# Kernel optimization log

Hardware: AMD Instinct MI355X
Metric: run time of the kernel (lower is better)

Reference implementation:

```python
import jax, jax.numpy as jnp
import numpy as np

N, E, D, R, L = 100000, 800000, 64, 7, 3
HID, KH = D // 4, 32          # IEConv hidden = dims[i]//4, kernel_hidden_dim = 32
EDGE_DIM = 14
BN_EPS = 1e-5
LN_EPS = 1e-5


def _normalize(v, eps=1e-12):
    n = jnp.linalg.norm(v, axis=-1, keepdims=True)
    return v / jnp.maximum(n, eps)


def _bn(h, p):
    # eval-mode BatchNorm1d; p: [4, dim] = (gamma, beta, running_mean, running_var)
    return (h - p[2]) * jax.lax.rsqrt(p[3] + BN_EPS) * p[0] + p[1]


def setup_inputs() -> dict:
    key = jax.random.key(0)
    keys = iter(jax.random.split(key, 40))
    nk = lambda: next(keys)
    par = lambda shape, s=0.1: jax.random.normal(nk(), shape, jnp.float32) * s

    def bn_par(dim):
        g = 1.0 + 0.1 * jax.random.normal(nk(), (L, dim), jnp.float32)
        b = 0.1 * jax.random.normal(nk(), (L, dim), jnp.float32)
        m = 0.1 * jax.random.normal(nk(), (L, dim), jnp.float32)
        v = 0.5 + jax.random.uniform(nk(), (L, dim), jnp.float32)
        return jnp.stack([g, b, m, v], axis=1)  # [L,4,dim]

    inp = {
        "x": jax.random.normal(nk(), (N, D), jnp.float32),
        "pos": jax.random.normal(nk(), (N, 3), jnp.float32) * 10.0,
        "edge_index": jax.random.randint(nk(), (2, E), 0, N),
        "edge_relation": jax.random.randint(nk(), (E,), 0, R),
        # GeometricRelationalGraphConv params (per layer)
        "W_rel": par((L, R * D, D)), "b_rel": par((L, D)),
        "W_self": par((L, D, D)), "b_self": par((L, D)),
        # IEConvLayer params
        "W_l1": par((L, D, HID)), "b_l1": par((L, HID)),
        "W_k1": par((L, EDGE_DIM, KH)), "b_k1": par((L, KH)),
        "W_k2": par((L, KH, (HID + 1) * HID)), "b_k2": par((L, (HID + 1) * HID)),
        "W_l2": par((L, HID, D)), "b_l2": par((L, D)),
        "bn_in": bn_par(D), "bn_msg": bn_par(HID), "bn_upd": bn_par(HID), "bn_out": bn_par(D),
        "ln_g": 1.0 + 0.1 * jax.random.normal(nk(), (L, D), jnp.float32),
        "ln_b": 0.1 * jax.random.normal(nk(), (L, D), jnp.float32),
    }
    return inp


def _forward(x, pos, W_rel, b_rel, W_self, b_self, W_l1, b_l1, W_k1, b_k1,
             W_k2, b_k2, W_l2, b_l2, bn_in, bn_msg, bn_upd, bn_out, ln_g, ln_b,
             edge_index, edge_relation):
    node_in, node_out = edge_index[0], edge_index[1]
    # ---- get_ieconv_edge_feature ----
    ones3 = jnp.ones((1, 3), x.dtype)
    u = _normalize(jnp.concatenate([ones3, pos[1:] - pos[:-1]], axis=0))        # [N,3]
    b = _normalize(jnp.concatenate([u[:-1] - u[1:], ones3], axis=0))
    n = _normalize(jnp.concatenate([jnp.cross(u[:-1], u[1:]), ones3], axis=0))
    frame = jnp.stack([b, n, jnp.cross(b, n)], axis=-1)                          # [N,3,3]
    t = jnp.einsum('ejk,ej->ek', frame[node_in], pos[node_out] - pos[node_in])  # [E,3]
    r = jnp.sum(frame[node_in] * frame[node_out], axis=1)                        # [E,3]
    delta = (jnp.abs(node_in - node_out).astype(x.dtype) / 6.0)[:, None]         # atom2residue = arange
    edge_feat = jnp.concatenate(
        [t, r, delta, 1 - 2 * jnp.abs(t), 1 - 2 * jnp.abs(r), 1 - 2 * jnp.abs(delta)], axis=-1)  # [E,14]

    deg = jnp.maximum(
        jax.ops.segment_sum(jnp.ones_like(node_out, dtype=x.dtype), node_out, num_segments=N), 1.0)[:, None]
    seg = node_out * R + edge_relation
    h = x
    for i in range(L):
        # GeometricRelationalGraphConv: relation-bucketed scatter-sum, per-relation linear + self loop, relu
        upd = jax.ops.segment_sum(h[node_in], seg, num_segments=N * R).reshape(N, R * h.shape[-1])
        rel_out = jax.nn.relu(upd @ W_rel[i] + b_rel[i] + h @ W_self[i] + b_self[i])
        # IEConvLayer (eval mode, dropouts identity)
        li = jax.nn.relu(_bn(h, bn_in[i]))
        m = jax.nn.relu(_bn(li[node_in] @ W_l1[i] + b_l1[i], bn_msg[i]))         # [E,HID]
        ker = (jax.nn.relu(edge_feat @ W_k1[i] + b_k1[i]) @ W_k2[i] + b_k2[i]).reshape(-1, HID + 1, HID)
        m = jnp.einsum('ejk,ej->ek', ker[:, 1:, :], m) + ker[:, 0, :]            # per-edge kernel conv
        upd2 = jax.ops.segment_sum(m, node_out, num_segments=N) / deg            # scatter-mean
        upd2 = jax.nn.relu(_bn(upd2, bn_upd[i]))
        ie_out = _bn(upd2 @ W_l2[i] + b_l2[i], bn_out[i])
        hidden = rel_out + ie_out + h  # short_cut: shapes match at every layer
        mu = jnp.mean(hidden, axis=-1, keepdims=True)
        var = jnp.var(hidden, axis=-1, keepdims=True)
        h = (hidden - mu) * jax.lax.rsqrt(var + LN_EPS) * ln_g[i] + ln_b[i]
    return h


def reference(x, pos, edge_index, edge_relation, W_rel, b_rel, W_self, b_self,
              W_l1, b_l1, W_k1, b_k1, W_k2, b_k2, W_l2, b_l2,
              bn_in, bn_msg, bn_upd, bn_out, ln_g, ln_b):
    return _forward(x, pos, W_rel, b_rel, W_self, b_self, W_l1, b_l1, W_k1, b_k1,
                    W_k2, b_k2, W_l2, b_l2, bn_in, bn_msg, bn_upd, bn_out, ln_g, ln_b,
                    edge_index, edge_relation)
```

## Files before the change

### kernel.cpp

```cpp
#include <hip/hip_runtime.h>
#include <hip/hip_bf16.h>

typedef unsigned short u16;
typedef unsigned int   u32;

static const int Nn  = 100000;
static const int Ne  = 800000;
static const int Ll  = 3;
static const int SCAN_B = 98;

typedef short     short8  __attribute__((ext_vector_type(8)));
typedef float     floatx4 __attribute__((ext_vector_type(4)));

static const int H_CUM[19] = {
  0, 86016, 86208, 98496, 98688, 101760, 101808, 103152, 103248,
  129360, 130176, 133248, 133440, 134208, 134400, 134592, 135360, 135552, 135744
};
static const int H_SZ[18] = {
  86016, 192, 12288, 192, 3072, 48, 1344, 96,
  26112, 816, 3072, 192, 768, 192, 192, 768, 192, 192
};

union FU { u32 u; float f; };
__device__ __forceinline__ float b2f(u16 v) { FU x; x.u = ((u32)v) << 16; return x.f; }
__device__ __forceinline__ float lo2f(u32 w) { FU x; x.u = w << 16; return x.f; }
__device__ __forceinline__ float hi2f(u32 w) { FU x; x.u = w & 0xffff0000u; return x.f; }
__device__ __forceinline__ u16 f2b(float f) {
  FU x; x.f = f;
  u32 u = x.u;
  u32 r = (u + 0x7FFFu + ((u >> 16) & 1u)) >> 16;
  return (u16)r;
}
__device__ __forceinline__ u32 pk2(float a, float b) {
  __hip_bfloat162 h2 = __float22bfloat162_rn(make_float2(a, b));
  union { __hip_bfloat162 h; u32 u; } c; c.h = h2; return c.u;
}

__global__ void k_bnprep(const float* __restrict__ W, float* __restrict__ bnAB) {
  int idx = blockIdx.x * blockDim.x + threadIdx.x;
  if (idx >= 480) return;
  int i = idx / 160, d0 = idx % 160;
  const float* src; float* dstA; float* dstB; int dim, d;
  if (d0 < 64)       { d = d0;      src = W + 133440 + i * 256; dim = 64; dstA = bnAB + i*320 + 0;   dstB = bnAB + i*320 + 64;  }
  else if (d0 < 80)  { d = d0 - 64; src = W + 134208 + i * 64;  dim = 16; dstA = bnAB + i*320 + 128; dstB = bnAB + i*320 + 144; }
  else if (d0 < 96)  { d = d0 - 80; src = W + 134400 + i * 64;  dim = 16; dstA = bnAB + i*320 + 160; dstB = bnAB + i*320 + 176; }
  else               { d = d0 - 96; src = W + 134592 + i * 256; dim = 64; dstA = bnAB + i*320 + 192; dstB = bnAB + i*320 + 256; }
  float g = src[0*dim+d], b = src[1*dim+d], m = src[2*dim+d], v = src[3*dim+d];
  float A = g * rsqrtf(v + 1e-5f);
  float B = b - m * A;
  dstA[d] = A; dstB[d] = B;
}

__global__ void k_prep(const float* __restrict__ W, u16* __restrict__ BswG) {
  int i = blockIdx.x * 256 + threadIdx.x;
  if (i >= 3 * 8704) return;
  int layer = i / 8704, r = i % 8704;
  int jp = r / 512, l2 = r % 512;
  int lane = l2 / 8, j = l2 % 8;
  int q = (lane >> 4) * 8 + j, n = lane & 15;
  const float* Wk2 = W + 103248 + layer * 8704;
  BswG[i] = f2b(Wk2[q * 272 + jp * 16 + n]);
}

__global__ void k_prep2(const float* __restrict__ W, u16* __restrict__ B2) {
  int idx = blockIdx.x * 256 + threadIdx.x;
  if (idx >= 3 * 65536) return;
  int layer = idx >> 16, r = idx & 65535;
  int fr = r >> 9;
  int lane = (r >> 3) & 63, j = r & 7;
  int hl = fr & 1, ks = (fr >> 1) & 1, nt = (fr >> 2) & 3, nc = fr >> 4;
  int k = ks * 32 + (lane >> 4) * 8 + j;
  int g = nc * 64 + nt * 16 + (lane & 15);
  const float* Wrel  = W + layer * 28672;
  const float* Wself = W + 86208 + layer * 4096;
  float v = (g < 448) ? Wrel[((g >> 6) * 64 + k) * 64 + (g & 63)]
                      : Wself[k * 64 + (g - 448)];
  u16 hi = f2b(v);
  B2[idx] = hl ? f2b(v - b2f(hi)) : hi;
}

__global__ void k_u(const float* __restrict__ posf, float* __restrict__ u) {
  int i = blockIdx.x * blockDim.x + threadIdx.x;
  if (i >= Nn) return;
  float ux, uy, uz;
  if (i == 0) { ux = uy = uz = 0.57735026918962584f; }
  else {
    float vx = posf[i*3+0] - posf[(i-1)*3+0];
    float vy = posf[i*3+1] - posf[(i-1)*3+1];
    float vz = posf[i*3+2] - posf[(i-1)*3+2];
    float nrm = sqrtf(vx*vx + vy*vy + vz*vz);
    float inv = 1.0f / fmaxf(nrm, 1e-12f);
    ux = vx*inv; uy = vy*inv; uz = vz*inv;
  }
  u[i*3+0] = ux; u[i*3+1] = uy; u[i*3+2] = uz;
}

__global__ void k_frame(const float* __restrict__ u, float* __restrict__ frame) {
  int i = blockIdx.x * blockDim.x + threadIdx.x;
  if (i >= Nn) return;
  float bx, by, bz, nx, ny, nz;
  if (i < Nn - 1) {
    float ax = u[i*3+0], ay = u[i*3+1], az = u[i*3+2];
    float cx = u[(i+1)*3+0], cy = u[(i+1)*3+1], cz = u[(i+1)*3+2];
    float dx = ax-cx, dy = ay-cy, dz = az-cz;
    float n1 = sqrtf(dx*dx + dy*dy + dz*dz);
    float i1 = 1.0f / fmaxf(n1, 1e-12f);
    bx = dx*i1; by = dy*i1; bz = dz*i1;
    float qx = ay*cz - az*cy, qy = az*cx - ax*cz, qz = ax*cy - ay*cx;
    float n2 = sqrtf(qx*qx + qy*qy + qz*qz);
    float i2 = 1.0f / fmaxf(n2, 1e-12f);
    nx = qx*i2; ny = qy*i2; nz = qz*i2;
  } else {
    bx = by = bz = 0.57735026918962584f;
    nx = ny = nz = 0.57735026918962584f;
  }
  float ex = by*nz - bz*ny, ey = bz*nx - bx*nz, ez = bx*ny - by*nx;
  frame[i*9+0] = bx; frame[i*9+1] = nx; frame[i*9+2] = ex;
  frame[i*9+3] = by; frame[i*9+4] = ny; frame[i*9+5] = ey;
  frame[i*9+6] = bz; frame[i*9+7] = nz; frame[i*9+8] = ez;
}

__global__ void k_edge(const int* __restrict__ EI, const float* __restrict__ posf,
                       const float* __restrict__ frame,
                       float* __restrict__ t0, float* __restrict__ t1, float* __restrict__ t2,
                       float* __restrict__ r0, float* __restrict__ r1, float* __restrict__ r2,
                       int* __restrict__ cnt) {
  int e = blockIdx.x * 256 + threadIdx.x;
  int vin = EI[e], vout = EI[Ne + e];
  float fi[9], fo[9];
#pragma unroll
  for (int t = 0; t < 9; t++) fi[t] = frame[(size_t)vin*9 + t];
#pragma unroll
  for (int t = 0; t < 9; t++) fo[t] = frame[(size_t)vout*9 + t];
  float d0 = posf[vout*3+0] - posf[vin*3+0];
  float d1 = posf[vout*3+1] - posf[vin*3+1];
  float d2 = posf[vout*3+2] - posf[vin*3+2];
  float tt[3], rr[3];
#pragma unroll
  for (int k = 0; k < 3; k++) {
    tt[k] = fi[0*3+k]*d0 + fi[1*3+k]*d1 + fi[2*3+k]*d2;
    rr[k] = fi[0*3+k]*fo[0*3+k] + fi[1*3+k]*fo[1*3+k] + fi[2*3+k]*fo[2*3+k];
  }
  t0[e] = tt[0]; t1[e] = tt[1]; t2[e] = tt[2];
  r0[e] = rr[0]; r1[e] = rr[1]; r2[e] = rr[2];
  atomicAdd(&cnt[vout], 1);
}

__global__ __launch_bounds__(1024) void k_scan1(const int* __restrict__ cnt,
                                                int* __restrict__ locExc,
                                                int* __restrict__ btot) {
  __shared__ int sm[1024];
  int t = threadIdx.x, b = blockIdx.x;
  int i = b * 1024 + t;
  int v = (i < Nn) ? cnt[i] : 0;
  sm[t] = v;
  __syncthreads();
#pragma unroll
  for (int off = 1; off < 1024; off <<= 1) {
    int x = (t >= off) ? sm[t - off] : 0;
    __syncthreads();
    sm[t] += x;
    __syncthreads();
  }
  if (i < Nn) locExc[i] = sm[t] - v;
  if (t == 1023) btot[b] = sm[1023];
}

__global__ void k_scan2(const int* __restrict__ btot, int* __restrict__ boff,
                        int* __restrict__ rowptr) {
  if (threadIdx.x != 0 || blockIdx.x != 0) return;
  int run = 0;
  for (int b = 0; b < SCAN_B; b++) { boff[b] = run; run += btot[b]; }
  rowptr[Nn] = run;
}

__global__ void k_scan3(const int* __restrict__ cnt, const int* __restrict__ locExc,
                        const int* __restrict__ boff, int* __restrict__ rowptr,
                        float* __restrict__ deginv) {
  int i = blockIdx.x * blockDim.x + threadIdx.x;
  if (i >= Nn) return;
  rowptr[i] = locExc[i] + boff[i >> 10];
  int dv = cnt[i] > 1 ? cnt[i] : 1;
  deginv[i] = 1.0f / (float)dv;
}

__global__ void k_place(const int* __restrict__ EI, const int* __restrict__ EREL,
                        const int* __restrict__ rowptr,
                        int* __restrict__ fill, int* __restrict__ yidx,
                        int* __restrict__ inv) {
  int e = blockIdx.x * blockDim.x + threadIdx.x;
  if (e >= Ne) return;
  int vout = EI[Ne + e];
  int p = atomicAdd(&fill[vout], 1);
  int slot = rowptr[vout] + p;
  inv[e] = slot;
  yidx[slot] = EI[e] * 448 + EREL[e] * 64;
}

__global__ __launch_bounds__(256) void k_rel2(
    const float* __restrict__ h, const u16* __restrict__ Bsw,
    const float* __restrict__ brel, const float* __restrict__ bself,
    u16* __restrict__ Y, u16* __restrict__ S) {
  __shared__ uint4 bs4[1024];
  int tid = threadIdx.x;
  int w = tid >> 6, lane = tid & 63;
  int kq = lane >> 4, cl = lane & 15;
  int nb0 = blockIdx.x * 64;
  int anode = nb0 + w * 16 + cl;
  union U { uint4 u; short8 v; };

  uint4 Ah[2], Al[2];
#pragma unroll
  for (int ks = 0; ks < 2; ks++) {
    float p[8] = {0.f,0.f,0.f,0.f,0.f,0.f,0.f,0.f};
    if (anode < Nn) {
      const float4* hp = (const float4*)(h + (size_t)anode * 64 + ks * 32 + kq * 8);
      float4 q0 = hp[0], q1 = hp[1];
      p[0]=q0.x; p[1]=q0.y; p[2]=q0.z; p[3]=q0.w;
      p[4]=q1.x; p[5]=q1.y; p[6]=q1.z; p[7]=q1.w;
    }
    u32 hw[4], lw[4];
#pragma unroll
    for (int t = 0; t < 4; t++) {
      u16 ha = f2b(p[2*t]), hb = f2b(p[2*t+1]);
      hw[t] = (u32)ha | ((u32)hb << 16);
      lw[t] = pk2(p[2*t] - b2f(ha), p[2*t+1] - b2f(hb));
    }
    Ah[ks] = make_uint4(hw[0], hw[1], hw[2], hw[3]);
    Al[ks] = make_uint4(lw[0], lw[1], lw[2], lw[3]);
  }

  for (int nc = 0; nc < 8; nc++) {
    if (nc) __syncthreads();
    const uint4* src = (const uint4*)(Bsw + nc * 8192);
#pragma unroll
    for (int i = 0; i < 4; i++) bs4[tid + i * 256] = src[tid + i * 256];
    __syncthreads();

    floatx4 acc[4];
#pragma unroll
    for (int nt = 0; nt < 4; nt++) acc[nt] = (floatx4){0.f, 0.f, 0.f, 0.f};
#pragma unroll
    for (int nt = 0; nt < 4; nt++) {
#pragma unroll
      for (int ks = 0; ks < 2; ks++) {
        U bh, bl, ah, al;
        bh.u = bs4[((nt*2 + ks)*2 + 0)*64 + lane];
        bl.u = bs4[((nt*2 + ks)*2 + 1)*64 + lane];
        ah.u = Ah[ks]; al.u = Al[ks];
        acc[nt] = __builtin_amdgcn_mfma_f32_16x16x32_bf16(ah.v, bh.v, acc[nt], 0, 0, 0);
        acc[nt] = __builtin_amdgcn_mfma_f32_16x16x32_bf16(al.v, bh.v, acc[nt], 0, 0, 0);
        acc[nt] = __builtin_amdgcn_mfma_f32_16x16x32_bf16(ah.v, bl.v, acc[nt], 0, 0, 0);
      }
    }
    if (nc < 7) {
#pragma unroll
      for (int nt = 0; nt < 4; nt++) {
#pragma unroll
        for (int reg = 0; reg < 4; reg++) {
          int node = nb0 + w * 16 + kq * 4 + reg;
          if (node < Nn)
            Y[(size_t)node * 448 + nc * 64 + nt * 16 + cl] = f2b(acc[nt][reg]);
        }
      }
    } else {
#pragma unroll
      for (int nt = 0; nt < 4; nt++) {
        int c = nt * 16 + cl;
        float bias = brel[c] + bself[c];
#pragma unroll
        for (int reg = 0; reg < 4; reg++) {
          int node = nb0 + w * 16 + kq * 4 + reg;
          if (node < Nn)
            S[(size_t)node * 64 + c] = f2b(acc[nt][reg] + bias);
        }
      }
    }
  }
}

__global__ __launch_bounds__(256) void k_z(
    const float* __restrict__ h, const float* __restrict__ Wl1, const float* __restrict__ bl1,
    const float* __restrict__ bk2, const float* __restrict__ bn,
    u16* __restrict__ zt, u16* __restrict__ biast) {
  __shared__ float ls[64][65];
  __shared__ float zz[64][17];
  int tid = threadIdx.x;
  int nb0 = blockIdx.x * 64;
  const float* Ain = bn + 0;
  const float* Bin = bn + 64;
#pragma unroll
  for (int r = 0; r < 16; r++) {
    int idx = r * 256 + tid;
    int row = idx >> 6, col = idx & 63;
    int node = nb0 + row;
    float v = (node < Nn) ? h[(size_t)node * 64 + col] : 0.0f;
    ls[row][col] = fmaxf(v * Ain[col] + Bin[col], 0.0f);
  }
  __syncthreads();
  int row = tid >> 2, jq = (tid & 3) * 4;
  int node = nb0 + row;
  const float* Amsg = bn + 128;
  const float* Bmsg = bn + 144;
  float m1[4];
#pragma unroll
  for (int t = 0; t < 4; t++) m1[t] = bl1[jq + t];
  for (int c = 0; c < 64; c++) {
    float lv = ls[row][c];
#pragma unroll
    for (int t = 0; t < 4; t++) m1[t] += lv * Wl1[c * 16 + jq + t];
  }
  float zv[4];
#pragma unroll
  for (int t = 0; t < 4; t++) {
    zv[t] = fmaxf(m1[t] * Amsg[jq + t] + Bmsg[jq + t], 0.0f);
    zz[row][jq + t] = zv[t];
  }
  if (node < Nn) {
    u32* zg = (u32*)zt + (size_t)node * 8 + (tid & 3) * 2;
    zg[0] = pk2(zv[0], zv[1]);
    zg[1] = pk2(zv[2], zv[3]);
  }
  __syncthreads();
  float bb[4];
#pragma unroll
  for (int t = 0; t < 4; t++) bb[t] = bk2[jq + t];
  for (int j = 0; j < 16; j++) {
    float zj = zz[row][j];
#pragma unroll
    for (int t = 0; t < 4; t++) bb[t] += zj * bk2[(j + 1) * 16 + jq + t];
  }
  if (node < Nn) {
    u32* bg = (u32*)biast + (size_t)node * 8 + (tid & 3) * 2;
    bg[0] = pk2(bb[0], bb[1]);
    bg[1] = pk2(bb[2], bb[3]);
  }
}

__global__ __launch_bounds__(256) void k_msg(
    const float* __restrict__ t0, const float* __restrict__ t1, const float* __restrict__ t2,
    const float* __restrict__ r0, const float* __restrict__ r1, const float* __restrict__ r2,
    const int* __restrict__ EI, const int* __restrict__ inv,
    const u16* __restrict__ zt, const u16* __restrict__ biast,
    const float* __restrict__ Wk1, const float* __restrict__ bk1,
    const u16* __restrict__ BswG, u16* __restrict__ mo) {
  __shared__ u16 abuf[256 * 72];
  __shared__ u32 bsw[4352];

  int tid = threadIdx.x;
  int e0 = blockIdx.x * 256;
  int e = e0 + tid;

  for (int i = tid; i < 4352; i += 256) bsw[i] = ((const u32*)BswG)[i];

  int vin = EI[e], vout = EI[Ne + e];

  {
    const uint4* zg = (const uint4*)(zt + (size_t)vin * 16);
    uint4* zr = (uint4*)(abuf + (size_t)tid * 72 + 32);
    zr[0] = zg[0]; zr[1] = zg[1];
    const uint4* bg = (const uint4*)(biast + (size_t)vin * 16);
    uint4* br = (uint4*)(abuf + (size_t)tid * 72 + 48);
    br[0] = bg[0]; br[1] = bg[1];
  }

  float ef[14];
  ef[0] = t0[e]; ef[1] = t1[e]; ef[2] = t2[e];
  ef[3] = r0[e]; ef[4] = r1[e]; ef[5] = r2[e];
  int ad = vin - vout; if (ad < 0) ad = -ad;
  ef[6] = ((float)ad) / 6.0f;
#pragma unroll
  for (int k = 0; k < 7; k++) ef[7+k] = 1.0f - 2.0f*fabsf(ef[k]);

  float a[32];
#pragma unroll
  for (int q = 0; q < 32; q++) a[q] = bk1[q];
#pragma unroll
  for (int d = 0; d < 14; d++) {
    float fv = ef[d];
#pragma unroll
    for (int q = 0; q < 32; q++) a[q] += fv * Wk1[d*32 + q];
  }
  u32* ar = (u32*)(abuf + (size_t)tid * 72);
#pragma unroll
  for (int q = 0; q < 16; q++)
    ar[q] = pk2(fmaxf(a[2*q], 0.0f), fmaxf(a[2*q+1], 0.0f));
  __syncthreads();

  int lane = tid & 63, w4 = (tid >> 6) * 4;
  int m = lane & 15, quad = lane >> 4;
  union U { uint4 u; short8 v; };
#pragma unroll
  for (int t = 0; t < 4; t++) {
    int s0 = (w4 + t) * 16;
    int s = s0 + m;
    const u16* rs = abuf + (size_t)s * 72;
    U afr;
    afr.u = *(const uint4*)(rs + quad * 8);
    const u32* aw = (const u32*)&afr.u;
    float av[8];
#pragma unroll
    for (int j = 0; j < 4; j++) { av[2*j] = lo2f(aw[j]); av[2*j+1] = hi2f(aw[j]); }

    uint4 zu0 = *(const uint4*)(rs + 32);
    uint4 zu1 = *(const uint4*)(rs + 40);
    const u32* zw0 = (const u32*)&zu0;
    const u32* zw1 = (const u32*)&zu1;
    float zf[16];
#pragma unroll
    for (int j = 0; j < 4; j++) {
      zf[2*j]   = lo2f(zw0[j]); zf[2*j+1]   = hi2f(zw0[j]);
      zf[8+2*j] = lo2f(zw1[j]); zf[8+2*j+1] = hi2f(zw1[j]);
    }

    floatx4 acc = {0.0f, 0.0f, 0.0f, 0.0f};
    U bfr;
    bfr.u = *(const uint4*)(bsw + (size_t)(0 * 64 + lane) * 4);
    acc = __builtin_amdgcn_mfma_f32_16x16x32_bf16(afr.v, bfr.v, acc, 0, 0, 0);

#pragma unroll
    for (int jp = 1; jp < 17; jp++) {
      float zv = zf[jp - 1];
      U pf;
      u32* pw = (u32*)&pf.u;
#pragma unroll
      for (int j = 0; j < 4; j++)
        pw[j] = pk2(av[2*j] * zv, av[2*j+1] * zv);
      bfr.u = *(const uint4*)(bsw + (size_t)(jp * 64 + lane) * 4);
      acc = __builtin_amdgcn_mfma_f32_16x16x32_bf16(pf.v, bfr.v, acc, 0, 0, 0);
    }

    int k = m;
#pragma unroll
    for (int reg = 0; reg < 4; reg++) {
      int se = s0 + quad * 4 + reg;
      float bias = b2f(abuf[(size_t)se * 72 + 48 + k]);
      int slot = inv[e0 + se];
      mo[(size_t)slot * 16 + k] = f2b(acc[reg] + bias);
    }
  }
}

__global__ __launch_bounds__(256) void k_node(
    const float* __restrict__ h, const u16* __restrict__ S, const u16* __restrict__ Y,
    const int* __restrict__ rowptr, const int* __restrict__ yidx,
    const u16* __restrict__ mo, const float* __restrict__ deginv,
    const float* __restrict__ Wl2, const float* __restrict__ bl2,
    const float* __restrict__ bn, const float* __restrict__ lng, const float* __restrict__ lnb,
    float* __restrict__ hout) {
  __shared__ float relsm[4][64];
  __shared__ float u2s[4][16];
  int tid = threadIdx.x;
  int lane = tid & 63, w = tid >> 6;
  int n = blockIdx.x * 4 + w;
  bool act = (n < Nn);

  if (act) {
    int beg = rowptr[n], end = rowptr[n+1];

    int g = lane >> 4, col4 = lane & 15;
    float a4[4] = {0.f, 0.f, 0.f, 0.f};
    for (int c0 = beg; c0 < end; c0 += 64) {
      int l = c0 + lane;
      int yo = (l < end) ? yidx[l] : 0;
      int cnt = end - c0; if (cnt > 64) cnt = 64;
      for (int j0 = 0; j0 < cnt; j0 += 4) {
        int j = j0 + g;
        int yoj = __shfl(yo, j, 64);
        if (j < cnt) {
          uint2 d = *(const uint2*)(Y + (size_t)yoj + col4 * 4);
          a4[0] += lo2f(d.x); a4[1] += hi2f(d.x);
          a4[2] += lo2f(d.y); a4[3] += hi2f(d.y);
        }
      }
    }
#pragma unroll
    for (int t = 0; t < 4; t++) {
      a4[t] += __shfl_xor(a4[t], 16, 64);
      a4[t] += __shfl_xor(a4[t], 32, 64);
    }
    if (lane < 16) {
#pragma unroll
      for (int t = 0; t < 4; t++) relsm[w][col4 * 4 + t] = a4[t];
    }

    int r = lane >> 2, c4 = lane & 3;
    float p4[4] = {0.f, 0.f, 0.f, 0.f};
    for (int p0 = beg; p0 < end; p0 += 16) {
      int p = p0 + r;
      if (p < end) {
        uint2 d = *(const uint2*)(mo + (size_t)p * 16 + c4 * 4);
        p4[0] += lo2f(d.x); p4[1] += hi2f(d.x);
        p4[2] += lo2f(d.y); p4[3] += hi2f(d.y);
      }
    }
#pragma unroll
    for (int t = 0; t < 4; t++) {
      p4[t] += __shfl_xor(p4[t],  4, 64);
      p4[t] += __shfl_xor(p4[t],  8, 64);
      p4[t] += __shfl_xor(p4[t], 16, 64);
      p4[t] += __shfl_xor(p4[t], 32, 64);
    }
    const float* Aupd = bn + 160;
    const float* Bupd = bn + 176;
    if (lane < 4) {
      float di = deginv[n];
#pragma unroll
      for (int t = 0; t < 4; t++) {
        int col = c4 * 4 + t;
        float v = p4[t] * di;
        u2s[w][col] = fmaxf(v * Aupd[col] + Bupd[col], 0.0f);
      }
    }
  }
  __syncthreads();
  if (act) {
    float rel_out = fmaxf(b2f(S[(size_t)n*64 + lane]) + relsm[w][lane], 0.0f);
    float ie = bl2[lane];
#pragma unroll
    for (int j = 0; j < 16; j++) ie += u2s[w][j] * Wl2[j*64 + lane];
    const float* Aout = bn + 192;
    const float* Bout = bn + 256;
    ie = ie * Aout[lane] + Bout[lane];
    float hidden = rel_out + ie + h[(size_t)n*64 + lane];
    float s = hidden;
#pragma unroll
    for (int off = 32; off > 0; off >>= 1) s += __shfl_xor(s, off, 64);
    float mu = s * (1.0f/64.0f);
    float d = hidden - mu;
    float s2 = d * d;
#pragma unroll
    for (int off = 32; off > 0; off >>= 1) s2 += __shfl_xor(s2, off, 64);
    float var = s2 * (1.0f/64.0f);
    float o = d * rsqrtf(var + 1e-5f) * lng[lane] + lnb[lane];
    hout[(size_t)n*64 + lane] = o;
  }
}

extern "C" void kernel_launch(void* const* d_in, const int* in_sizes, int n_in,
                              void* d_out, int out_size, void* d_ws, size_t ws_size,
                              hipStream_t stream) {
  const float* x    = (const float*)d_in[0];
  const float* posf = (const float*)d_in[1];
  const int* EI     = (const int*)d_in[2];
  const int* EREL   = (const int*)d_in[3];
  float* outf       = (float*)d_out;

  char* p = (char*)d_ws;
  auto alloc = [&](size_t bytes) -> char* {
    char* r = p;
    p += (bytes + 255) & ~((size_t)255);
    return r;
  };
  float* W      = (float*)alloc((size_t)135744 * 4);
  float* bnAB   = (float*)alloc((size_t)960 * 4);
  u16*   BswG   = (u16*)  alloc((size_t)3 * 8704 * 2);
  u16*   Bsw2   = (u16*)  alloc((size_t)3 * 65536 * 2);
  float* u      = (float*)alloc((size_t)Nn * 3 * 4);
  float* frame  = (float*)alloc((size_t)Nn * 9 * 4);
  int*   cnt    = (int*)  alloc((size_t)Nn * 4);
  int*   fill   = (int*)  alloc((size_t)Nn * 4);
  int*   rowptr = (int*)  alloc((size_t)(Nn + 1) * 4);
  int*   locExc = (int*)  alloc((size_t)Nn * 4);
  int*   btot   = (int*)  alloc((size_t)SCAN_B * 4);
  int*   boff   = (int*)  alloc((size_t)SCAN_B * 4);
  int*   yidx   = (int*)  alloc((size_t)Ne * 4);
  int*   inv    = (int*)  alloc((size_t)Ne * 4);
  float* deginv = (float*)alloc((size_t)Nn * 4);
  float* h      = (float*)alloc((size_t)Nn * 64 * 4);
  u16*   S      = (u16*)  alloc((size_t)Nn * 64 * 2);
  u16*   Y      = (u16*)  alloc((size_t)Nn * 448 * 2);
  u16*   mo     = (u16*)  alloc((size_t)Ne * 16 * 2);
  u16*   zt     = (u16*)  alloc((size_t)Nn * 16 * 2);
  u16*   biast  = (u16*)  alloc((size_t)Nn * 16 * 2);
  float* et0    = (float*)alloc((size_t)Ne * 4);
  float* et1    = (float*)alloc((size_t)Ne * 4);
  float* et2    = (float*)alloc((size_t)Ne * 4);
  float* er0    = (float*)alloc((size_t)Ne * 4);
  float* er1    = (float*)alloc((size_t)Ne * 4);
  float* er2    = (float*)alloc((size_t)Ne * 4);
  (void)n_in; (void)in_sizes; (void)out_size;

  size_t needed = (size_t)(p - (char*)d_ws);
  if (needed > ws_size) return;

  hipMemsetAsync(cnt,  0, (size_t)Nn * 4, stream);
  hipMemsetAsync(fill, 0, (size_t)Nn * 4, stream);

  for (int k = 0; k < 18; k++)
    hipMemcpyAsync(W + H_CUM[k], d_in[4 + k], (size_t)H_SZ[k] * 4,
                   hipMemcpyDeviceToDevice, stream);
  hipMemcpyAsync(h, x, (size_t)Nn * 64 * 4, hipMemcpyDeviceToDevice, stream);

  k_bnprep<<<2, 256, 0, stream>>>(W, bnAB);
  k_prep<<<(3*8704 + 255)/256, 256, 0, stream>>>(W, BswG);
  k_prep2<<<(3*65536 + 255)/256, 256, 0, stream>>>(W, Bsw2);
  k_u<<<(Nn + 255)/256, 256, 0, stream>>>(posf, u);
  k_frame<<<(Nn + 255)/256, 256, 0, stream>>>(u, frame);
  k_edge<<<Ne/256, 256, 0, stream>>>(EI, posf, frame, et0, et1, et2, er0, er1, er2, cnt);
  k_scan1<<<SCAN_B, 1024, 0, stream>>>(cnt, locExc, btot);
  k_scan2<<<1, 64, 0, stream>>>(btot, boff, rowptr);
  k_scan3<<<(Nn + 255)/256, 256, 0, stream>>>(cnt, locExc, boff, rowptr, deginv);
  k_place<<<Ne/256, 256, 0, stream>>>(EI, EREL, rowptr, fill, yidx, inv);

  for (int i = 0; i < Ll; i++) {
    const float* brel  = W + H_CUM[1]  + i * 64;
    const float* bself = W + H_CUM[3]  + i * 64;
    const float* Wl1   = W + H_CUM[4]  + i * 1024;
    const float* bl1   = W + H_CUM[5]  + i * 16;
    const float* Wk1   = W + H_CUM[6]  + i * 448;
    const float* bk1   = W + H_CUM[7]  + i * 32;
    const float* bk2   = W + H_CUM[9]  + i * 272;
    const float* Wl2   = W + H_CUM[10] + i * 1024;
    const float* bl2   = W + H_CUM[11] + i * 64;
    const float* lng   = W + H_CUM[16] + i * 64;
    const float* lnb   = W + H_CUM[17] + i * 64;
    const float* bnL   = bnAB + i * 320;
    const u16*   BswL  = BswG + i * 8704;

    k_rel2<<<(Nn + 63)/64, 256, 0, stream>>>(h, Bsw2 + i * 65536, brel, bself, Y, S);
    k_z<<<(Nn + 63)/64, 256, 0, stream>>>(h, Wl1, bl1, bk2, bnL, zt, biast);
    k_msg<<<Ne/256, 256, 0, stream>>>(et0, et1, et2, er0, er1, er2, EI, inv,
                                      zt, biast, Wk1, bk1, BswL, mo);
    k_node<<<(Nn + 3)/4, 256, 0, stream>>>(h, S, Y, rowptr, yidx, mo, deginv,
                                           Wl2, bl2, bnL, lng, lnb,
                                           (i == Ll - 1) ? outf : h);
  }
}
```

Baseline: 897.2 us.

## Move edge-kernel MLP first layer to MFMA and restructure per-edge conv contraction

The first kernel-MLP layer (14->32 FMA per edge in scalar code) is now computed with bf16 MFMAs, using a hi/lo split of the edge features and weights to keep near-fp32 accuracy. A new prep kernel packs Wk1 into MFMA fragments. The per-edge kernel conv is reordered so that 17 MFMAs produce the kernel matrix slices first, and the z-weighted sum is then done in fp32 per output register. This removes the per-step bf16 packing of products. It adds register pressure from holding 17 floatx4 accumulators and extra LDS round trips.

```diff
diff --git a/kernel.cpp b/kernel.cpp
--- a/kernel.cpp
+++ b/kernel.cpp
@@ -77,6 +77,29 @@
                       : Wself[k * 64 + (g - 448)];
   u16 hi = f2b(v);
   B2[idx] = hl ? f2b(v - b2f(hi)) : hi;
+}
+
+__global__ void k_prep3(const float* __restrict__ W, u16* __restrict__ Wk1f) {
+  int idx = blockIdx.x * 256 + threadIdx.x;
+  if (idx >= 3 * 2048) return;
+  int layer = idx / 2048, r = idx % 2048;
+  int kind = (r >> 10) & 1, nt = (r >> 9) & 1;
+  int lane = (r >> 3) & 63, j = r & 7;
+  int k = (lane >> 4) * 8 + j;
+  int q = nt * 16 + (lane & 15);
+  const float* Wk1 = W + 101808 + layer * 448;
+  u16 out = 0;
+  if (kind == 0) {
+    if (k < 14)       out = f2b(Wk1[k * 32 + q]);
+    else if (k < 28)  out = f2b(Wk1[(k - 14) * 32 + q]);
+  } else {
+    if (k < 14) {
+      float w = Wk1[k * 32 + q];
+      u16 hi = f2b(w);
+      out = f2b(w - b2f(hi));
+    }
+  }
+  Wk1f[idx] = out;
 }
 
 __global__ void k_u(const float* __restrict__ posf, float* __restrict__ u) {
@@ -342,7 +365,7 @@
     const float* __restrict__ r0, const float* __restrict__ r1, const float* __restrict__ r2,
     const int* __restrict__ EI, const int* __restrict__ inv,
     const u16* __restrict__ zt, const u16* __restrict__ biast,
-    const float* __restrict__ Wk1, const float* __restrict__ bk1,
+    const u16* __restrict__ Wk1f, const float* __restrict__ bk1,
     const u16* __restrict__ BswG, u16* __restrict__ mo) {
   __shared__ u16 abuf[256 * 72];
   __shared__ u32 bsw[4352];
@@ -372,71 +395,80 @@
 #pragma unroll
   for (int k = 0; k < 7; k++) ef[7+k] = 1.0f - 2.0f*fabsf(ef[k]);
 
-  float a[32];
-#pragma unroll
-  for (int q = 0; q < 32; q++) a[q] = bk1[q];
+  u16 row[32];
 #pragma unroll
   for (int d = 0; d < 14; d++) {
-    float fv = ef[d];
-#pragma unroll
-    for (int q = 0; q < 32; q++) a[q] += fv * Wk1[d*32 + q];
-  }
+    u16 hi = f2b(ef[d]);
+    row[d] = hi;
+    row[14 + d] = f2b(ef[d] - b2f(hi));
+  }
+#pragma unroll
+  for (int d = 28; d < 32; d++) row[d] = 0;
   u32* ar = (u32*)(abuf + (size_t)tid * 72);
 #pragma unroll
-  for (int q = 0; q < 16; q++)
-    ar[q] = pk2(fmaxf(a[2*q], 0.0f), fmaxf(a[2*q+1], 0.0f));
+  for (int i = 0; i < 16; i++)
+    ar[i] = (u32)row[2*i] | ((u32)row[2*i+1] << 16);
   __syncthreads();
 
   int lane = tid & 63, w4 = (tid >> 6) * 4;
   int m = lane & 15, quad = lane >> 4;
   union U { uint4 u; short8 v; };
+
+  U b0[2], b1[2];
+#pragma unroll
+  for (int nt = 0; nt < 2; nt++) {
+    b0[nt].u = *(const uint4*)(Wk1f + 0*1024 + nt*512 + lane*8);
+    b1[nt].u = *(const uint4*)(Wk1f + 1*1024 + nt*512 + lane*8);
+  }
+  float bk1v[2] = { bk1[m], bk1[16 + m] };
+
 #pragma unroll
   for (int t = 0; t < 4; t++) {
     int s0 = (w4 + t) * 16;
-    int s = s0 + m;
-    const u16* rs = abuf + (size_t)s * 72;
-    U afr;
-    afr.u = *(const uint4*)(rs + quad * 8);
-    const u32* aw = (const u32*)&afr.u;
-    float av[8];
-#pragma unroll
-    for (int j = 0; j < 4; j++) { av[2*j] = lo2f(aw[j]); av[2*j+1] = hi2f(aw[j]); }
-
-    uint4 zu0 = *(const uint4*)(rs + 32);
-    uint4 zu1 = *(const uint4*)(rs + 40);
-    const u32* zw0 = (const u32*)&zu0;
-    const u32* zw1 = (const u32*)&zu1;
-    float zf[16];
-#pragma unroll
-    for (int j = 0; j < 4; j++) {
-      zf[2*j]   = lo2f(zw0[j]); zf[2*j+1]   = hi2f(zw0[j]);
-      zf[8+2*j] = lo2f(zw1[j]); zf[8+2*j+1] = hi2f(zw1[j]);
-    }
-
-    floatx4 acc = {0.0f, 0.0f, 0.0f, 0.0f};
-    U bfr;
-    bfr.u = *(const uint4*)(bsw + (size_t)(0 * 64 + lane) * 4);
-    acc = __builtin_amdgcn_mfma_f32_16x16x32_bf16(afr.v, bfr.v, acc, 0, 0, 0);
-
-#pragma unroll
-    for (int jp = 1; jp < 17; jp++) {
-      float zv = zf[jp - 1];
-      U pf;
-      u32* pw = (u32*)&pf.u;
-#pragma unroll
-      for (int j = 0; j < 4; j++)
-        pw[j] = pk2(av[2*j] * zv, av[2*j+1] * zv);
-      bfr.u = *(const uint4*)(bsw + (size_t)(jp * 64 + lane) * 4);
-      acc = __builtin_amdgcn_mfma_f32_16x16x32_bf16(pf.v, bfr.v, acc, 0, 0, 0);
-    }
-
-    int k = m;
+    const u16* rs0 = abuf + (size_t)(s0 + m) * 72;
+
+    U efr; efr.u = *(const uint4*)(rs0 + quad * 8);
+#pragma unroll
+    for (int nt = 0; nt < 2; nt++) {
+      floatx4 aa = {0.f, 0.f, 0.f, 0.f};
+      aa = __builtin_amdgcn_mfma_f32_16x16x32_bf16(efr.v, b0[nt].v, aa, 0, 0, 0);
+      aa = __builtin_amdgcn_mfma_f32_16x16x32_bf16(efr.v, b1[nt].v, aa, 0, 0, 0);
+#pragma unroll
+      for (int reg = 0; reg < 4; reg++) {
+        int se = s0 + quad * 4 + reg;
+        float av = fmaxf(aa[reg] + bk1v[nt], 0.0f);
+        abuf[(size_t)se * 72 + nt * 16 + m] = f2b(av);
+      }
+    }
+
+    U afr; afr.u = *(const uint4*)(rs0 + quad * 8);
+    floatx4 ker[17];
+#pragma unroll
+    for (int jp = 0; jp < 17; jp++) {
+      U bfr; bfr.u = *(const uint4*)(bsw + (size_t)(jp * 64 + lane) * 4);
+      floatx4 z4 = {0.f, 0.f, 0.f, 0.f};
+      ker[jp] = __builtin_amdgcn_mfma_f32_16x16x32_bf16(afr.v, bfr.v, z4, 0, 0, 0);
+    }
+
 #pragma unroll
     for (int reg = 0; reg < 4; reg++) {
       int se = s0 + quad * 4 + reg;
-      float bias = b2f(abuf[(size_t)se * 72 + 48 + k]);
+      const u16* rz = abuf + (size_t)se * 72 + 32;
+      uint4 z0 = *(const uint4*)rz;
+      uint4 z1 = *(const uint4*)(rz + 8);
+      const u32* zw0 = (const u32*)&z0;
+      const u32* zw1 = (const u32*)&z1;
+      float acc = ker[0][reg];
+#pragma unroll
+      for (int j = 0; j < 4; j++) {
+        acc += lo2f(zw0[j]) * ker[1 + 2*j][reg];
+        acc += hi2f(zw0[j]) * ker[2 + 2*j][reg];
+        acc += lo2f(zw1[j]) * ker[9 + 2*j][reg];
+        acc += hi2f(zw1[j]) * ker[10 + 2*j][reg];
+      }
+      float bias = b2f(abuf[(size_t)se * 72 + 48 + m]);
       int slot = inv[e0 + se];
-      mo[(size_t)slot * 16 + k] = f2b(acc[reg] + bias);
+      mo[(size_t)slot * 16 + m] = f2b(acc + bias);
     }
   }
 }
@@ -556,6 +588,7 @@
   float* bnAB   = (float*)alloc((size_t)960 * 4);
   u16*   BswG   = (u16*)  alloc((size_t)3 * 8704 * 2);
   u16*   Bsw2   = (u16*)  alloc((size_t)3 * 65536 * 2);
+  u16*   Wk1f   = (u16*)  alloc((size_t)3 * 2048 * 2);
   float* u      = (float*)alloc((size_t)Nn * 3 * 4);
   float* frame  = (float*)alloc((size_t)Nn * 9 * 4);
   int*   cnt    = (int*)  alloc((size_t)Nn * 4);
@@ -595,6 +628,7 @@
   k_bnprep<<<2, 256, 0, stream>>>(W, bnAB);
   k_prep<<<(3*8704 + 255)/256, 256, 0, stream>>>(W, BswG);
   k_prep2<<<(3*65536 + 255)/256, 256, 0, stream>>>(W, Bsw2);
+  k_prep3<<<(3*2048 + 255)/256, 256, 0, stream>>>(W, Wk1f);
   k_u<<<(Nn + 255)/256, 256, 0, stream>>>(posf, u);
   k_frame<<<(Nn + 255)/256, 256, 0, stream>>>(u, frame);
   k_edge<<<Ne/256, 256, 0, stream>>>(EI, posf, frame, et0, et1, et2, er0, er1, er2, cnt);
@@ -608,7 +642,6 @@
     const float* bself = W + H_CUM[3]  + i * 64;
     const float* Wl1   = W + H_CUM[4]  + i * 1024;
     const float* bl1   = W + H_CUM[5]  + i * 16;
-    const float* Wk1   = W + H_CUM[6]  + i * 448;
     const float* bk1   = W + H_CUM[7]  + i * 32;
     const float* bk2   = W + H_CUM[9]  + i * 272;
     const float* Wl2   = W + H_CUM[10] + i * 1024;
@@ -621,7 +654,7 @@
     k_rel2<<<(Nn + 63)/64, 256, 0, stream>>>(h, Bsw2 + i * 65536, brel, bself, Y, S);
     k_z<<<(Nn + 63)/64, 256, 0, stream>>>(h, Wl1, bl1, bk2, bnL, zt, biast);
     k_msg<<<Ne/256, 256, 0, stream>>>(et0, et1, et2, er0, er1, er2, EI, inv,
-                                      zt, biast, Wk1, bk1, BswL, mo);
+                                      zt, biast, Wk1f + i * 2048, bk1, BswL, mo);
     k_node<<<(Nn + 3)/4, 256, 0, stream>>>(h, S, Y, rowptr, yidx, mo, deginv,
                                            Wl2, bl2, bnL, lng, lnb,
                                            (i == Ll - 1) ? outf : h);
```

New measurement: 900.7 us. Within noise of the previous version (+0.4%).
